# Optimization experiments

Measured on AMD Instinct MI355X. Metric: run time of the kernel, lower is better.

Reference implementation:

```python
import jax, jax.numpy as jnp
import numpy as np

B, S, D = 4, 2048, 1024
H, DK, DV = 16, 64, 64


def setup_inputs() -> dict:
    key = jax.random.key(0)
    ks = jax.random.split(key, 7)
    scale = 0.02
    emb = jax.random.normal(ks[0], (B, S, D), dtype=jnp.float32)
    # per-head projection weights stacked over heads: [H, D, DK/DV]
    Wq = jax.random.normal(ks[1], (H, D, DK), dtype=jnp.float32) * scale
    Wk = jax.random.normal(ks[2], (H, D, DK), dtype=jnp.float32) * scale
    Wv = jax.random.normal(ks[3], (H, D, DV), dtype=jnp.float32) * scale
    # output projection (nn.Linear(d_model, d_model)): weight [D, D] (input-major) + bias
    Wo = jax.random.normal(ks[4], (D, D), dtype=jnp.float32) * scale
    bo = jax.random.normal(ks[5], (D,), dtype=jnp.float32) * scale
    return {"emb": emb, "Wq": Wq, "Wk": Wk, "Wv": Wv, "Wo": Wo, "bo": bo}


def reference(emb, Wq, Wk, Wv, Wo, bo):
    # Per-head projections, batched over heads: [B,H,S,dk]
    q = jnp.einsum("bsd,hdk->bhsk", emb, Wq)
    k = jnp.einsum("bsd,hdk->bhsk", emb, Wk)
    v = jnp.einsum("bsd,hdv->bhsv", emb, Wv)
    # Scaled dot-product with causal mask (bool_mask=True)
    scores = jnp.einsum("bhqk,bhsk->bhqs", q, k) * (DK ** -0.5)  # [B,H,S,S]
    causal = jnp.tril(jnp.ones((S, S), dtype=bool))
    scores = jnp.where(causal, scores, jnp.finfo(scores.dtype).min)
    attn = jax.nn.softmax(scores, axis=-1)
    out = jnp.einsum("bhqs,bhsv->bhqv", attn, v)  # [B,H,S,DV]
    # concat heads -> [B,S,H*DV] == [B,S,D]
    out = out.transpose(0, 2, 1, 3).reshape(B, S, H * DV)
    # output projection; dropout=0.0 -> identity
    return out @ Wo + bo
```

## Files before the change

kernel.cpp:

```cpp
#include <hip/hip_runtime.h>
#include <hip/hip_bf16.h>


typedef __attribute__((ext_vector_type(8))) short bf16x8;
typedef __attribute__((ext_vector_type(4))) float f32x4;
typedef __attribute__((ext_vector_type(4))) unsigned int u32x4;
typedef __attribute__((ext_vector_type(2))) unsigned int u32x2;

#define MFMA16(a, b, c) __builtin_amdgcn_mfma_f32_16x16x32_bf16((a), (b), (c), 0, 0, 0)

#define LOG2E 1.44269504088896340736f
#define BIG_NEG (-3.0e38f)
#define DEFER_THR 10.0f

__device__ __forceinline__ unsigned short f2bf(float f) {
  union { float f; unsigned int i; } x; x.f = f;
  unsigned int lsb = (x.i >> 16) & 1;
  x.i += 0x7fffu + lsb;
  return (unsigned short)(x.i >> 16);
}

__device__ __forceinline__ unsigned int cvtpk(float lo, float hi) {
  unsigned int r;
  asm("v_cvt_pk_bf16_f32 %0, %1, %2" : "=v"(r) : "v"(lo), "v"(hi));
  return r;
}

__global__ void wtrans_kernel(const float* __restrict__ in,
                              unsigned short* __restrict__ out, int R, int C) {
  __shared__ unsigned short tile[32][33];
  const int bz = blockIdx.z;
  const int c0 = blockIdx.x * 32, r0 = blockIdx.y * 32;
  const float* ip = in + (size_t)bz * R * C;
  unsigned short* op = out + (size_t)bz * R * C;
  const int tx = threadIdx.x, ty = threadIdx.y;
#pragma unroll
  for (int i = 0; i < 32; i += 8)
    tile[ty + i][tx] = f2bf(ip[(size_t)(r0 + ty + i) * C + (c0 + tx)]);
  __syncthreads();
#pragma unroll
  for (int i = 0; i < 32; i += 8)
    op[(size_t)(c0 + ty + i) * R + (r0 + tx)] = tile[tx][ty + i];
}

__global__ __launch_bounds__(256)
void embconv_kernel(const float* __restrict__ in, unsigned short* __restrict__ out) {
  const int i = blockIdx.x * 256 + threadIdx.x;
  const float4 a = ((const float4*)in)[2 * i];
  const float4 b = ((const float4*)in)[2 * i + 1];
  union { unsigned short u[8]; u32x4 v; } p;
  p.u[0] = f2bf(a.x); p.u[1] = f2bf(a.y); p.u[2] = f2bf(a.z); p.u[3] = f2bf(a.w);
  p.u[4] = f2bf(b.x); p.u[5] = f2bf(b.y); p.u[6] = f2bf(b.z); p.u[7] = f2bf(b.w);
  ((u32x4*)out)[i] = p.v;
}

__global__ __launch_bounds__(256)
void qkv_kernel(const unsigned short* __restrict__ embB,
                const unsigned short* __restrict__ WqT,
                const unsigned short* __restrict__ WkT,
                const unsigned short* __restrict__ WvT,
                unsigned short* __restrict__ QG,
                unsigned short* __restrict__ KG,
                unsigned short* __restrict__ VtG) {
  const int t = blockIdx.z;
  const int m0 = blockIdx.y * 128;
  const int n0 = blockIdx.x * 128;
  const int b = m0 >> 11;
  const int sloc = m0 & 2047;
  const unsigned short* Wt =
      (t == 0 ? WqT : (t == 1 ? WkT : WvT)) + (size_t)(n0 >> 6) * 64 * 1024;

  __shared__ __align__(16) unsigned short As[128][40];
  __shared__ __align__(16) unsigned short Bs[128][40];

  const int tid = threadIdx.x;
  const int lane = tid & 63, w = tid >> 6;
  const int q4 = lane >> 4, l16 = lane & 15;
  const int arow = tid >> 1, acol = (tid & 1) * 16;

  f32x4 acc[4][4] = {};

  for (int k0 = 0; k0 < 1024; k0 += 32) {
    __syncthreads();
    *(u32x4*)&As[arow][acol]     = *(const u32x4*)&embB[(size_t)(m0 + arow) * 1024 + k0 + acol];
    *(u32x4*)&As[arow][acol + 8] = *(const u32x4*)&embB[(size_t)(m0 + arow) * 1024 + k0 + acol + 8];
    *(u32x4*)&Bs[arow][acol]     = *(const u32x4*)&Wt[(size_t)arow * 1024 + k0 + acol];
    *(u32x4*)&Bs[arow][acol + 8] = *(const u32x4*)&Wt[(size_t)arow * 1024 + k0 + acol + 8];
    __syncthreads();

    const unsigned short (*PA)[40] = (t == 2) ? Bs : As;
    const unsigned short (*PB)[40] = (t == 2) ? As : Bs;

    bf16x8 af[4], bfr[4];
#pragma unroll
    for (int ms = 0; ms < 4; ++ms)
      af[ms] = *(const bf16x8*)&PA[(w >> 1) * 64 + ms * 16 + l16][q4 * 8];
#pragma unroll
    for (int js = 0; js < 4; ++js)
      bfr[js] = *(const bf16x8*)&PB[(w & 1) * 64 + js * 16 + l16][q4 * 8];
#pragma unroll
    for (int ms = 0; ms < 4; ++ms)
#pragma unroll
      for (int js = 0; js < 4; ++js)
        acc[ms][js] = MFMA16(af[ms], bfr[js], acc[ms][js]);
  }

  if (t < 2) {
    unsigned short* outp = (t == 0) ? QG : KG;
    const float osc = (t == 0) ? (0.125f * LOG2E) : 1.0f;
    const int h = (n0 >> 6) + (w & 1);
    const size_t hb = (size_t)(b * 16 + h) * 2048;
#pragma unroll
    for (int ms = 0; ms < 4; ++ms)
#pragma unroll
      for (int js = 0; js < 4; ++js) {
        const int c = js * 16 + l16;
#pragma unroll
        for (int r = 0; r < 4; ++r) {
          const int s = sloc + (w >> 1) * 64 + ms * 16 + q4 * 4 + r;
          outp[(hb + s) * 64 + c] = f2bf(acc[ms][js][r] * osc);
        }
      }
  } else {
    const int h = (n0 >> 6) + (w >> 1);
    const size_t hb = (size_t)(b * 16 + h) * 64;
#pragma unroll
    for (int ms = 0; ms < 4; ++ms)
#pragma unroll
      for (int js = 0; js < 4; ++js) {
        const int s = sloc + (w & 1) * 64 + js * 16 + l16;
#pragma unroll
        for (int r = 0; r < 4; ++r) {
          const int c = ms * 16 + q4 * 4 + r;
          VtG[(hb + c) * 2048 + s] = f2bf(acc[ms][js][r]);
        }
      }
  }
}

__global__ __launch_bounds__(512)
void flash_kernel(const unsigned short* __restrict__ QG,
                  const unsigned short* __restrict__ KG,
                  const unsigned short* __restrict__ VtG,
                  unsigned short* __restrict__ ObG) {
  const int bh = blockIdx.y;
  const int x = blockIdx.x;
  const int q0B = (31 - x) * 64;
  const int tid = threadIdx.x;
  const int lane = tid & 63, w = tid >> 6;
  const int wp = w & 3;
  const int q0w = (w < 4) ? q0B : x * 64;
  const int q4 = lane >> 4, l16 = lane & 15;

  const unsigned short* Qp = QG + ((size_t)bh * 2048 + q0w + wp * 16) * 64;
  const unsigned short* Kp = KG + (size_t)bh * 2048 * 64;
  const unsigned short* Vp = VtG + (size_t)bh * 64 * 2048;

  const bf16x8 qf0 = *(const bf16x8*)&Qp[(size_t)l16 * 64 + q4 * 8];
  const bf16x8 qf1 = *(const bf16x8*)&Qp[(size_t)l16 * 64 + 32 + q4 * 8];

  __shared__ __align__(16) unsigned short Ks[64][72];
  __shared__ __align__(16) unsigned short Vs[64][72];
  __shared__ __align__(16) unsigned short Plds[8][16][72];

  f32x4 oacc[4] = {};
  float m_i = BIG_NEG, l_i = 0.f;

  const int sr = tid >> 3, sc = (tid & 7) * 8;
  u32x4 kreg = *(const u32x4*)&Kp[(size_t)sr * 64 + sc];
  u32x4 vreg = *(const u32x4*)&Vp[(size_t)sr * 2048 + sc];

  for (int j0 = 0; j0 <= q0B; j0 += 64) {
    *(u32x4*)&Ks[sr][sc] = kreg;
    *(u32x4*)&Vs[sr][sc] = vreg;
    __syncthreads();

    if (j0 + 64 <= q0B) {
      const int jn = j0 + 64;
      kreg = *(const u32x4*)&Kp[(size_t)(jn + sr) * 64 + sc];
      vreg = *(const u32x4*)&Vp[(size_t)sr * 2048 + jn + sc];
    }

    if (j0 <= q0w) {
      f32x4 sacc[4] = {};
#pragma unroll
      for (int js = 0; js < 4; ++js) {
        const bf16x8 kf0 = *(const bf16x8*)&Ks[js * 16 + l16][q4 * 8];
        const bf16x8 kf1 = *(const bf16x8*)&Ks[js * 16 + l16][32 + q4 * 8];
        sacc[js] = MFMA16(kf0, qf0, sacc[js]);
        sacc[js] = MFMA16(kf1, qf1, sacc[js]);
      }

      float mloc = BIG_NEG;
      if (j0 == q0w) {
        const int qrel = wp * 16 + l16;
#pragma unroll
        for (int js = 0; js < 4; ++js)
#pragma unroll
          for (int r = 0; r < 4; ++r) {
            const int krel = js * 16 + q4 * 4 + r;
            float v = sacc[js][r];
            if (krel > qrel) v = BIG_NEG;
            sacc[js][r] = v;
            mloc = fmaxf(mloc, v);
          }
      } else {
#pragma unroll
        for (int js = 0; js < 4; ++js)
#pragma unroll
          for (int r = 0; r < 4; ++r) mloc = fmaxf(mloc, sacc[js][r]);
      }
      mloc = fmaxf(mloc, __shfl_xor(mloc, 16, 64));
      mloc = fmaxf(mloc, __shfl_xor(mloc, 32, 64));

      if (__any(mloc > m_i + DEFER_THR)) {
        const float mnew = fmaxf(m_i, mloc);
        const float alpha = __builtin_amdgcn_exp2f(m_i - mnew);
        m_i = mnew;
        l_i *= alpha;
#pragma unroll
        for (int js = 0; js < 4; ++js)
#pragma unroll
          for (int r = 0; r < 4; ++r) oacc[js][r] *= alpha;
      }

      float sm = 0.f;
#pragma unroll
      for (int js = 0; js < 4; ++js)
#pragma unroll
        for (int r = 0; r < 4; ++r) {
          const float p = __builtin_amdgcn_exp2f(sacc[js][r] - m_i);
          sacc[js][r] = p;
          sm += p;
        }
      sm += __shfl_xor(sm, 16, 64);
      sm += __shfl_xor(sm, 32, 64);
      l_i += sm;

#pragma unroll
      for (int js = 0; js < 4; ++js) {
        u32x2 pk;
        pk[0] = cvtpk(sacc[js][0], sacc[js][1]);
        pk[1] = cvtpk(sacc[js][2], sacc[js][3]);
        *(u32x2*)&Plds[w][l16][js * 16 + q4 * 4] = pk;
      }

      asm volatile("" ::: "memory");

      const bf16x8 pf0 = *(const bf16x8*)&Plds[w][l16][q4 * 8];
      const bf16x8 pf1 = *(const bf16x8*)&Plds[w][l16][32 + q4 * 8];

#pragma unroll
      for (int js = 0; js < 4; ++js) {
        const bf16x8 vf0 = *(const bf16x8*)&Vs[js * 16 + l16][q4 * 8];
        const bf16x8 vf1 = *(const bf16x8*)&Vs[js * 16 + l16][32 + q4 * 8];
        oacc[js] = MFMA16(vf0, pf0, oacc[js]);
        oacc[js] = MFMA16(vf1, pf1, oacc[js]);
      }
    }
    __syncthreads();
  }

  const int b = bh >> 4, h = bh & 15;
  const int q = q0w + wp * 16 + l16;
  const float rl = 1.0f / l_i;
  unsigned short* orow = ObG + ((size_t)b * 2048 + q) * 1024 + h * 64;
#pragma unroll
  for (int js = 0; js < 4; ++js) {
    u32x2 ok;
    ok[0] = cvtpk(oacc[js][0] * rl, oacc[js][1] * rl);
    ok[1] = cvtpk(oacc[js][2] * rl, oacc[js][3] * rl);
    *(u32x2*)&orow[js * 16 + q4 * 4] = ok;
  }
}

__global__ __launch_bounds__(256)
void oproj_kernel(const unsigned short* __restrict__ ObG,
                  const unsigned short* __restrict__ WoT,
                  const float* __restrict__ bo,
                  float* __restrict__ outG) {
  const int m0 = blockIdx.y * 128;
  const int n0 = blockIdx.x * 128;

  __shared__ __align__(16) unsigned short As[128][40];
  __shared__ __align__(16) unsigned short Bs[128][40];

  const int tid = threadIdx.x;
  const int lane = tid & 63, w = tid >> 6;
  const int q4 = lane >> 4, l16 = lane & 15;
  const int arow = tid >> 1, acol = (tid & 1) * 16;

  f32x4 acc[4][4] = {};

  for (int k0 = 0; k0 < 1024; k0 += 32) {
    __syncthreads();
    *(u32x4*)&As[arow][acol]     = *(const u32x4*)&ObG[(size_t)(m0 + arow) * 1024 + k0 + acol];
    *(u32x4*)&As[arow][acol + 8] = *(const u32x4*)&ObG[(size_t)(m0 + arow) * 1024 + k0 + acol + 8];
    *(u32x4*)&Bs[arow][acol]     = *(const u32x4*)&WoT[(size_t)(n0 + arow) * 1024 + k0 + acol];
    *(u32x4*)&Bs[arow][acol + 8] = *(const u32x4*)&WoT[(size_t)(n0 + arow) * 1024 + k0 + acol + 8];
    __syncthreads();

    bf16x8 af[4], bfr[4];
#pragma unroll
    for (int ms = 0; ms < 4; ++ms)
      af[ms] = *(const bf16x8*)&As[(w >> 1) * 64 + ms * 16 + l16][q4 * 8];
#pragma unroll
    for (int js = 0; js < 4; ++js)
      bfr[js] = *(const bf16x8*)&Bs[(w & 1) * 64 + js * 16 + l16][q4 * 8];
#pragma unroll
    for (int ms = 0; ms < 4; ++ms)
#pragma unroll
      for (int js = 0; js < 4; ++js)
        acc[ms][js] = MFMA16(af[ms], bfr[js], acc[ms][js]);
  }

#pragma unroll
  for (int js = 0; js < 4; ++js) {
    const int col = n0 + (w & 1) * 64 + js * 16 + l16;
    const float bias = bo[col];
#pragma unroll
    for (int ms = 0; ms < 4; ++ms)
#pragma unroll
      for (int r = 0; r < 4; ++r) {
        const int row = m0 + (w >> 1) * 64 + ms * 16 + q4 * 4 + r;
        outG[(size_t)row * 1024 + col] = acc[ms][js][r] + bias;
      }
  }
}

extern "C" void kernel_launch(void* const* d_in, const int* in_sizes, int n_in,
                              void* d_out, int out_size, void* d_ws, size_t ws_size,
                              hipStream_t stream) {
  const float* emb = (const float*)d_in[0];
  const float* Wq  = (const float*)d_in[1];
  const float* Wk  = (const float*)d_in[2];
  const float* Wv  = (const float*)d_in[3];
  const float* Wo  = (const float*)d_in[4];
  const float* bo  = (const float*)d_in[5];
  float* out = (float*)d_out;

  char* ws = (char*)d_ws;
  const size_t MB = 1024 * 1024;

  const int nb = (ws_size >= 72 * MB) ? 4 : (ws_size >= 40 * MB) ? 2 : 1;

  unsigned short* WqT = (unsigned short*)(ws + 0 * MB);
  unsigned short* WkT = (unsigned short*)(ws + 2 * MB);
  unsigned short* WvT = (unsigned short*)(ws + 4 * MB);
  unsigned short* WoT = (unsigned short*)(ws + 6 * MB);
  unsigned short* QG  = (unsigned short*)(ws + 8 * MB);
  unsigned short* KG  = (unsigned short*)(ws + (8 + 4 * nb) * MB);
  unsigned short* VtG = (unsigned short*)(ws + (8 + 8 * nb) * MB);
  unsigned short* ObG = (unsigned short*)(ws + (8 + 12 * nb) * MB);

  const dim3 tb(32, 8, 1);
  wtrans_kernel<<<dim3(2, 32, 16), tb, 0, stream>>>(Wq, WqT, 1024, 64);
  wtrans_kernel<<<dim3(2, 32, 16), tb, 0, stream>>>(Wk, WkT, 1024, 64);
  wtrans_kernel<<<dim3(2, 32, 16), tb, 0, stream>>>(Wv, WvT, 1024, 64);
  wtrans_kernel<<<dim3(32, 32, 1), tb, 0, stream>>>(Wo, WoT, 1024, 1024);

  for (int g = 0; g < 4; g += nb) {
    const float* embG = emb + (size_t)g * 2048 * 1024;
    float* outG = out + (size_t)g * 2048 * 1024;
    unsigned short* embB = ObG;
    embconv_kernel<<<dim3(nb * 1024), 256, 0, stream>>>(embG, embB);
    qkv_kernel<<<dim3(8, 16 * nb, 3), 256, 0, stream>>>(embB, WqT, WkT, WvT, QG, KG, VtG);
    flash_kernel<<<dim3(16, 16 * nb), 512, 0, stream>>>(QG, KG, VtG, ObG);
    oproj_kernel<<<dim3(8, 16 * nb), 256, 0, stream>>>(ObG, WoT, bo, outG);
  }
}
```

Measured before the change: 304.3 us.

## Register-prefetch GEMM tiles, raise MFMA priority, and swap flash grid axes

The QKV and output-projection GEMMs now load the next K-slice from global memory into registers while the current slice is computed from shared memory, which hides global load latency behind the MFMAs. MFMA blocks in all three kernels are wrapped in s_setprio so compute-issuing waves get scheduler priority. The flash attention grid swaps its x/y axes so that consecutive blocks cover different heads for the same query tile, which changes dispatch order and load balance across the causal workload. The cost is extra registers for the prefetch buffers, which could lower occupancy.

```diff
diff --git a/kernel.cpp b/kernel.cpp
--- a/kernel.cpp
+++ b/kernel.cpp
@@ -80,13 +80,26 @@
 
   f32x4 acc[4][4] = {};
 
+  const unsigned short* aptr = &embB[(size_t)(m0 + arow) * 1024 + acol];
+  const unsigned short* bptr = &Wt[(size_t)arow * 1024 + acol];
+  u32x4 a0 = *(const u32x4*)&aptr[0];
+  u32x4 a1 = *(const u32x4*)&aptr[8];
+  u32x4 b0 = *(const u32x4*)&bptr[0];
+  u32x4 b1 = *(const u32x4*)&bptr[8];
+
   for (int k0 = 0; k0 < 1024; k0 += 32) {
-    __syncthreads();
-    *(u32x4*)&As[arow][acol]     = *(const u32x4*)&embB[(size_t)(m0 + arow) * 1024 + k0 + acol];
-    *(u32x4*)&As[arow][acol + 8] = *(const u32x4*)&embB[(size_t)(m0 + arow) * 1024 + k0 + acol + 8];
-    *(u32x4*)&Bs[arow][acol]     = *(const u32x4*)&Wt[(size_t)arow * 1024 + k0 + acol];
-    *(u32x4*)&Bs[arow][acol + 8] = *(const u32x4*)&Wt[(size_t)arow * 1024 + k0 + acol + 8];
-    __syncthreads();
+    *(u32x4*)&As[arow][acol]     = a0;
+    *(u32x4*)&As[arow][acol + 8] = a1;
+    *(u32x4*)&Bs[arow][acol]     = b0;
+    *(u32x4*)&Bs[arow][acol + 8] = b1;
+    __syncthreads();
+
+    if (k0 + 32 < 1024) {
+      a0 = *(const u32x4*)&aptr[k0 + 32];
+      a1 = *(const u32x4*)&aptr[k0 + 40];
+      b0 = *(const u32x4*)&bptr[k0 + 32];
+      b1 = *(const u32x4*)&bptr[k0 + 40];
+    }
 
     const unsigned short (*PA)[40] = (t == 2) ? Bs : As;
     const unsigned short (*PB)[40] = (t == 2) ? As : Bs;
@@ -98,11 +111,14 @@
 #pragma unroll
     for (int js = 0; js < 4; ++js)
       bfr[js] = *(const bf16x8*)&PB[(w & 1) * 64 + js * 16 + l16][q4 * 8];
+    __builtin_amdgcn_s_setprio(1);
 #pragma unroll
     for (int ms = 0; ms < 4; ++ms)
 #pragma unroll
       for (int js = 0; js < 4; ++js)
         acc[ms][js] = MFMA16(af[ms], bfr[js], acc[ms][js]);
+    __builtin_amdgcn_s_setprio(0);
+    __syncthreads();
   }
 
   if (t < 2) {
@@ -143,8 +159,8 @@
                   const unsigned short* __restrict__ KG,
                   const unsigned short* __restrict__ VtG,
                   unsigned short* __restrict__ ObG) {
-  const int bh = blockIdx.y;
-  const int x = blockIdx.x;
+  const int bh = blockIdx.x;
+  const int x = blockIdx.y;
   const int q0B = (31 - x) * 64;
   const int tid = threadIdx.x;
   const int lane = tid & 63, w = tid >> 6;
@@ -183,6 +199,7 @@
 
     if (j0 <= q0w) {
       f32x4 sacc[4] = {};
+      __builtin_amdgcn_s_setprio(1);
 #pragma unroll
       for (int js = 0; js < 4; ++js) {
         const bf16x8 kf0 = *(const bf16x8*)&Ks[js * 16 + l16][q4 * 8];
@@ -190,6 +207,7 @@
         sacc[js] = MFMA16(kf0, qf0, sacc[js]);
         sacc[js] = MFMA16(kf1, qf1, sacc[js]);
       }
+      __builtin_amdgcn_s_setprio(0);
 
       float mloc = BIG_NEG;
       if (j0 == q0w) {
@@ -250,6 +268,7 @@
       const bf16x8 pf0 = *(const bf16x8*)&Plds[w][l16][q4 * 8];
       const bf16x8 pf1 = *(const bf16x8*)&Plds[w][l16][32 + q4 * 8];
 
+      __builtin_amdgcn_s_setprio(1);
 #pragma unroll
       for (int js = 0; js < 4; ++js) {
         const bf16x8 vf0 = *(const bf16x8*)&Vs[js * 16 + l16][q4 * 8];
@@ -257,6 +276,7 @@
         oacc[js] = MFMA16(vf0, pf0, oacc[js]);
         oacc[js] = MFMA16(vf1, pf1, oacc[js]);
       }
+      __builtin_amdgcn_s_setprio(0);
     }
     __syncthreads();
   }
@@ -292,13 +312,26 @@
 
   f32x4 acc[4][4] = {};
 
+  const unsigned short* aptr = &ObG[(size_t)(m0 + arow) * 1024 + acol];
+  const unsigned short* bptr = &WoT[(size_t)(n0 + arow) * 1024 + acol];
+  u32x4 a0 = *(const u32x4*)&aptr[0];
+  u32x4 a1 = *(const u32x4*)&aptr[8];
+  u32x4 b0 = *(const u32x4*)&bptr[0];
+  u32x4 b1 = *(const u32x4*)&bptr[8];
+
   for (int k0 = 0; k0 < 1024; k0 += 32) {
-    __syncthreads();
-    *(u32x4*)&As[arow][acol]     = *(const u32x4*)&ObG[(size_t)(m0 + arow) * 1024 + k0 + acol];
-    *(u32x4*)&As[arow][acol + 8] = *(const u32x4*)&ObG[(size_t)(m0 + arow) * 1024 + k0 + acol + 8];
-    *(u32x4*)&Bs[arow][acol]     = *(const u32x4*)&WoT[(size_t)(n0 + arow) * 1024 + k0 + acol];
-    *(u32x4*)&Bs[arow][acol + 8] = *(const u32x4*)&WoT[(size_t)(n0 + arow) * 1024 + k0 + acol + 8];
-    __syncthreads();
+    *(u32x4*)&As[arow][acol]     = a0;
+    *(u32x4*)&As[arow][acol + 8] = a1;
+    *(u32x4*)&Bs[arow][acol]     = b0;
+    *(u32x4*)&Bs[arow][acol + 8] = b1;
+    __syncthreads();
+
+    if (k0 + 32 < 1024) {
+      a0 = *(const u32x4*)&aptr[k0 + 32];
+      a1 = *(const u32x4*)&aptr[k0 + 40];
+      b0 = *(const u32x4*)&bptr[k0 + 32];
+      b1 = *(const u32x4*)&bptr[k0 + 40];
+    }
 
     bf16x8 af[4], bfr[4];
 #pragma unroll
@@ -307,11 +340,14 @@
 #pragma unroll
     for (int js = 0; js < 4; ++js)
       bfr[js] = *(const bf16x8*)&Bs[(w & 1) * 64 + js * 16 + l16][q4 * 8];
+    __builtin_amdgcn_s_setprio(1);
 #pragma unroll
     for (int ms = 0; ms < 4; ++ms)
 #pragma unroll
       for (int js = 0; js < 4; ++js)
         acc[ms][js] = MFMA16(af[ms], bfr[js], acc[ms][js]);
+    __builtin_amdgcn_s_setprio(0);
+    __syncthreads();
   }
 
 #pragma unroll
@@ -365,7 +401,7 @@
     unsigned short* embB = ObG;
     embconv_kernel<<<dim3(nb * 1024), 256, 0, stream>>>(embG, embB);
     qkv_kernel<<<dim3(8, 16 * nb, 3), 256, 0, stream>>>(embB, WqT, WkT, WvT, QG, KG, VtG);
-    flash_kernel<<<dim3(16, 16 * nb), 512, 0, stream>>>(QG, KG, VtG, ObG);
+    flash_kernel<<<dim3(16 * nb, 16), 512, 0, stream>>>(QG, KG, VtG, ObG);
     oproj_kernel<<<dim3(8, 16 * nb), 256, 0, stream>>>(ObG, WoT, bo, outG);
   }
 }
```

Measured after the change: 291.4 us. 4.2% less time.
